# Optimization experiments

Hardware: AMD Instinct MI355X
Metric: run time of the kernel (lower is better)

The kernel has to match this reference:

```python
import jax, jax.numpy as jnp
import numpy as np

N_NODES, N_EDGES, BATCH, F_IN, GENES = 65536, 262144, 2048, 78, 735
HEADS, HID = 8, 64            # gnn_out_dim = HEADS*HID = 512
GOUT = HEADS * HID
NEG_SLOPE = 0.2
BN_EPS = 1e-5


def setup_inputs() -> dict:
    key = jax.random.key(0)
    ks = jax.random.split(key, 24)
    sc = lambda k, shp, fan: (jax.random.normal(k, shp, jnp.float32) / np.sqrt(fan)).astype(jnp.float32)
    d = {}
    d["x"] = jax.random.normal(ks[0], (N_NODES, F_IN), jnp.float32)
    d["edge_index"] = jax.random.randint(ks[1], (2, N_EDGES), 0, N_NODES)
    d["batch"] = jnp.sort(jax.random.randint(ks[2], (N_NODES,), 0, BATCH))
    d["x_gen"] = jax.random.normal(ks[3], (BATCH, GENES), jnp.float32)
    # GATConv 1: in=78 -> heads*hid
    d["W1"] = sc(ks[4], (F_IN, GOUT), F_IN)
    d["att_src1"] = sc(ks[5], (HEADS, HID), HID)
    d["att_dst1"] = sc(ks[6], (HEADS, HID), HID)
    d["bias1"] = jnp.zeros((GOUT,), jnp.float32)
    # GATConv 2: in=512 -> heads*hid
    d["W2"] = sc(ks[7], (GOUT, GOUT), GOUT)
    d["att_src2"] = sc(ks[8], (HEADS, HID), HID)
    d["att_dst2"] = sc(ks[9], (HEADS, HID), HID)
    d["bias2"] = jnp.zeros((GOUT,), jnp.float32)
    # geno encoder: Linear(735,128) -> BN -> ReLU -> Linear(128,512) -> ReLU
    d["gW1"] = sc(ks[10], (GENES, 2 * HID), GENES)
    d["gb1"] = jnp.zeros((2 * HID,), jnp.float32)
    d["bn_gamma"] = jnp.ones((2 * HID,), jnp.float32)
    d["bn_beta"] = jnp.zeros((2 * HID,), jnp.float32)
    d["bn_mean"] = jnp.zeros((2 * HID,), jnp.float32)
    d["bn_var"] = jnp.ones((2 * HID,), jnp.float32)
    d["gW2"] = sc(ks[11], (2 * HID, GOUT), 2 * HID)
    d["gb2"] = jnp.zeros((GOUT,), jnp.float32)
    # fusion MLP: 1024 -> 256 -> 128 -> 1
    d["fW1"] = sc(ks[12], (2 * GOUT, 256), 2 * GOUT)
    d["fb1"] = jnp.zeros((256,), jnp.float32)
    d["fW2"] = sc(ks[13], (256, 128), 256)
    d["fb2"] = jnp.zeros((128,), jnp.float32)
    d["fW3"] = sc(ks[14], (128, 1), 128)
    d["fb3"] = jnp.zeros((1,), jnp.float32)
    return d


def gat_layer(x, edge_index, W, att_src, att_dst, bias):
    """PyG GATConv (concat=True, add_self_loops=True), eval mode (no dropout)."""
    N = x.shape[0]
    H, C = att_src.shape
    h = (x @ W).reshape(N, H, C)                      # [N,H,C]
    a_src = jnp.einsum('nhc,hc->nh', h, att_src)      # [N,H]
    a_dst = jnp.einsum('nhc,hc->nh', h, att_dst)      # [N,H]
    loop = jnp.arange(N)
    src = jnp.concatenate([edge_index[0], loop])      # [E+N]
    dst = jnp.concatenate([edge_index[1], loop])
    e = jax.nn.leaky_relu(a_src[src] + a_dst[dst], NEG_SLOPE)   # [E+N,H]
    # scatter-softmax over incoming edges per destination node
    e_max = jax.ops.segment_max(e, dst, num_segments=N)
    e = jnp.exp(e - e_max[dst])
    denom = jax.ops.segment_sum(e, dst, num_segments=N)
    alpha = e / (denom[dst] + 1e-16)                  # [E+N,H]
    msg = h[src] * alpha[:, :, None]                  # [E+N,H,C]
    out = jax.ops.segment_sum(msg, dst, num_segments=N)  # [N,H,C]
    return out.reshape(N, H * C) + bias


def global_mean_pool(x, batch, num_graphs):
    sums = jax.ops.segment_sum(x, batch, num_segments=num_graphs)
    cnt = jax.ops.segment_sum(jnp.ones((x.shape[0],), x.dtype), batch, num_segments=num_graphs)
    return sums / jnp.maximum(cnt, 1.0)[:, None]


def reference(x, edge_index, batch, x_gen,
              W1, att_src1, att_dst1, bias1,
              W2, att_src2, att_dst2, bias2,
              gW1, gb1, bn_gamma, bn_beta, bn_mean, bn_var, gW2, gb2,
              fW1, fb1, fW2, fb2, fW3, fb3):
    h = jax.nn.elu(gat_layer(x, edge_index, W1, att_src1, att_dst1, bias1))
    h = jax.nn.elu(gat_layer(h, edge_index, W2, att_src2, att_dst2, bias2))
    g = global_mean_pool(h, batch, BATCH)             # [B, 512]
    # genomic encoder (eval-mode BatchNorm with running stats)
    z = x_gen @ gW1 + gb1
    z = (z - bn_mean) * jax.lax.rsqrt(bn_var + BN_EPS) * bn_gamma + bn_beta
    z = jax.nn.relu(z)
    z = jax.nn.relu(z @ gW2 + gb2)                    # [B, 512]
    c = jnp.concatenate([g, z], axis=1)               # [B, 1024]
    c = jax.nn.relu(c @ fW1 + fb1)
    c = jax.nn.relu(c @ fW2 + fb2)
    return c @ fW3 + fb3                              # [B, 1]
```

## Files before the change

kernel.cpp:

```cpp
#include <hip/hip_runtime.h>
#include <hip/hip_bf16.h>
#include <cstdint>
#include <cstddef>

#define NN 65536
#define NE 262144
#define NB 2048
#define FIN 78
#define GOUTD 512

typedef __bf16 bf16x8 __attribute__((ext_vector_type(8)));
typedef float f32x4 __attribute__((ext_vector_type(4)));

__device__ __forceinline__ float leaky02(float x) { return x > 0.f ? x : 0.2f * x; }

__global__ void k_zero2(int* __restrict__ a, int* __restrict__ b) {
    int i = blockIdx.x * 256 + threadIdx.x;
    if (i < NN) { a[i] = 0; b[i] = 0; }
}

__global__ void k_hist(const int* __restrict__ dst, int* __restrict__ deg) {
    int i = blockIdx.x * 256 + threadIdx.x;
    if (i < NE) atomicAdd(&deg[dst[i]], 1);
}

__global__ void k_scan_block(const int* __restrict__ deg, int* __restrict__ ex, int* __restrict__ bsum) {
    __shared__ int s[256];
    int t = threadIdx.x; int g = blockIdx.x * 256 + t;
    int v = deg[g];
    s[t] = v; __syncthreads();
    for (int d = 1; d < 256; d <<= 1) {
        int x = (t >= d) ? s[t - d] : 0;
        __syncthreads();
        s[t] += x;
        __syncthreads();
    }
    ex[g] = s[t] - v;
    if (t == 255) bsum[blockIdx.x] = s[t];
}

__global__ void k_scan_bsum(int* __restrict__ bsum) {
    __shared__ int s[256];
    int t = threadIdx.x;
    int v = bsum[t]; s[t] = v; __syncthreads();
    for (int d = 1; d < 256; d <<= 1) {
        int x = (t >= d) ? s[t - d] : 0;
        __syncthreads();
        s[t] += x;
        __syncthreads();
    }
    bsum[t] = s[t] - v;
}

__global__ void k_scan_add(int* __restrict__ rowptr, const int* __restrict__ bsum) {
    int i = blockIdx.x * 256 + threadIdx.x;
    rowptr[i] += bsum[blockIdx.x];
    if (i == 0) rowptr[NN] = NE;
}

__global__ void k_scatter(const int* __restrict__ src, const int* __restrict__ dst,
                          const int* __restrict__ rowptr, int* __restrict__ fill,
                          int* __restrict__ colI) {
    int i = blockIdx.x * 256 + threadIdx.x;
    if (i < NE) {
        int d = dst[i];
        int pos = rowptr[d] + atomicAdd(&fill[d], 1);
        colI[pos] = src[i];
    }
}

__global__ void k_gbounds(const int* __restrict__ batch, int* __restrict__ gstart) {
    int i = blockIdx.x * 256 + threadIdx.x;
    if (i >= NN) return;
    int cur = batch[i];
    int prev = (i == 0) ? -1 : batch[i - 1];
    for (int b = prev + 1; b <= cur; ++b) gstart[b] = i;
    if (i == NN - 1) {
        for (int b = cur + 1; b <= NB; ++b) gstart[b] = NN;
    }
}

__global__ void k_cvt_all(const float* __restrict__ x, const float* __restrict__ W1,
                          const float* __restrict__ W2, __hip_bfloat16* __restrict__ xb,
                          __hip_bfloat16* __restrict__ w1t, __hip_bfloat16* __restrict__ w2t)
{
    int blk = blockIdx.x;
    if (blk < 16384) {
        int i = blk * 256 + threadIdx.x;
        int row = i >> 6;
        int c = (i & 63) << 1;
        float v0 = (c < FIN) ? x[(size_t)row * FIN + c] : 0.f;
        float v1 = (c + 1 < FIN) ? x[(size_t)row * FIN + c + 1] : 0.f;
        __hip_bfloat16 o[2];
        o[0] = __float2bfloat16(v0);
        o[1] = __float2bfloat16(v1);
        *(uint32_t*)&xb[(size_t)row * 128 + c] = *(const uint32_t*)o;
    } else if (blk < 16640) {
        int i = (blk - 16384) * 256 + threadIdx.x;
        int n = i >> 7, k = i & 127;
        w1t[i] = __float2bfloat16(k < FIN ? W1[(size_t)k * 512 + n] : 0.f);
    } else {
        int i = (blk - 16640) * 256 + threadIdx.x;
        int n = i >> 9, k = i & 511;
        w2t[i] = __float2bfloat16(W2[(size_t)k * 512 + n]);
    }
}

__global__ __launch_bounds__(256) void k_mfma_gemm(
    const __hip_bfloat16* __restrict__ A, const __hip_bfloat16* __restrict__ BT,
    __hip_bfloat16* __restrict__ C, int K,
    const float* __restrict__ att_src, const float* __restrict__ att_dst,
    float* __restrict__ a_src, float* __restrict__ a_dst)
{
    __shared__ __hip_bfloat16 smem[128 * 128];
    __hip_bfloat16* As = smem;
    __hip_bfloat16* Bs = smem + 128 * 64;
    int tid = threadIdx.x;
    int lane = tid & 63;
    int wave = tid >> 6;
    int id = blockIdx.x;
    int m0 = (((id >> 5) << 3) + (id & 7)) * 128;
    int n0 = ((id >> 3) & 3) * 128;
    int wm = (wave >> 1) * 64;
    int wn = (wave & 1) * 64;
    f32x4 acc[4][4] = {};

    int swz = lane & 7;

    for (int k0 = 0; k0 < K; k0 += 64) {
        #pragma unroll
        for (int c = 0; c < 4; ++c) {
            int off = c * 4096 + tid * 16;
            int r = off >> 7;
            int c16 = (off >> 4) & 7;
            int c16s = c16 ^ (r & 7);
            __builtin_amdgcn_global_load_lds(
                (const __attribute__((address_space(1))) void*)(A + (size_t)(m0 + r) * K + k0 + c16s * 8),
                (__attribute__((address_space(3))) void*)((char*)As + off), 16, 0, 0);
            __builtin_amdgcn_global_load_lds(
                (const __attribute__((address_space(1))) void*)(BT + (size_t)(n0 + r) * K + k0 + c16s * 8),
                (__attribute__((address_space(3))) void*)((char*)Bs + off), 16, 0, 0);
        }
        __syncthreads();
        #pragma unroll
        for (int kk = 0; kk < 64; kk += 32) {
            int c16r = (kk >> 3) + (lane >> 4);
            bf16x8 af[4], bfr[4];
            #pragma unroll
            for (int t = 0; t < 4; ++t) {
                int ra = wm + t * 16 + (lane & 15);
                int rb = wn + t * 16 + (lane & 15);
                af[t]  = *(const bf16x8*)((char*)As + ra * 128 + ((c16r ^ swz) << 4));
                bfr[t] = *(const bf16x8*)((char*)Bs + rb * 128 + ((c16r ^ swz) << 4));
            }
            #pragma unroll
            for (int i = 0; i < 4; ++i)
                #pragma unroll
                for (int j = 0; j < 4; ++j)
                    acc[i][j] = __builtin_amdgcn_mfma_f32_16x16x32_bf16(af[i], bfr[j], acc[i][j], 0, 0, 0);
        }
        __syncthreads();
    }

    int rowb = wm + ((lane >> 4) << 2);
    int colb = wn + (lane & 15);
    #pragma unroll
    for (int i = 0; i < 4; ++i) {
        #pragma unroll
        for (int j = 0; j < 4; ++j) {
            int cc = colb + j * 16;
            #pragma unroll
            for (int r = 0; r < 4; ++r) {
                int rr = rowb + i * 16 + r;
                int word = (cc >> 1) ^ (((rr >> 2) & 7) << 3);
                smem[rr * 128 + word * 2 + (cc & 1)] = __float2bfloat16(acc[i][j][r]);
            }
        }
    }
    __syncthreads();
    #pragma unroll
    for (int cc2 = 0; cc2 < 8; ++cc2) {
        int p = cc2 * 256 + tid;
        int rr = p >> 4;
        int c16 = p & 15;
        int x = ((rr >> 2) & 7) << 3;
        bf16x8 v = *(const bf16x8*)((char*)smem + rr * 256 + ((((c16 << 2) ^ x)) << 2));
        *(bf16x8*)(C + (size_t)(m0 + rr) * 512 + n0 + c16 * 8) = v;
        const float* sp = att_src + n0 + c16 * 8;
        const float* dp = att_dst + n0 + c16 * 8;
        float4 s0 = *(const float4*)sp, s1 = *(const float4*)(sp + 4);
        float4 d0 = *(const float4*)dp, d1 = *(const float4*)(dp + 4);
        float sv[8] = {s0.x, s0.y, s0.z, s0.w, s1.x, s1.y, s1.z, s1.w};
        float dv[8] = {d0.x, d0.y, d0.z, d0.w, d1.x, d1.y, d1.z, d1.w};
        float ps = 0.f, pd = 0.f;
        #pragma unroll
        for (int k = 0; k < 8; ++k) {
            float f = (float)v[k];
            ps = fmaf(f, sv[k], ps);
            pd = fmaf(f, dv[k], pd);
        }
        #pragma unroll
        for (int d = 1; d < 8; d <<= 1) {
            ps += __shfl_xor(ps, d);
            pd += __shfl_xor(pd, d);
        }
        if ((c16 & 7) == 0) {
            int head = (n0 >> 6) + (c16 >> 3);
            a_src[(size_t)(m0 + rr) * 8 + head] = ps;
            a_dst[(size_t)(m0 + rr) * 8 + head] = pd;
        }
    }
}

__global__ __launch_bounds__(256) void k_geno1(
    const float* __restrict__ x_gen, const float* __restrict__ gW1,
    const float* __restrict__ gb1, const float* __restrict__ bn_mean,
    const float* __restrict__ bn_var, const float* __restrict__ bn_gamma,
    const float* __restrict__ bn_beta, float* __restrict__ z1)
{
    __shared__ float rowS[2][736];
    __shared__ float part[2][128];
    int t = threadIdx.x;
    int row0 = blockIdx.x * 2;
    int c = t & 127;
    int kh = t >> 7;
    for (int i = t; i < 1470; i += 256)
        rowS[i >= 735][i >= 735 ? i - 735 : i] = x_gen[(size_t)row0 * 735 + i];
    __syncthreads();
    int k0 = kh ? 368 : 0;
    int k1 = kh ? 735 : 368;
    float a0 = 0.f, a1 = 0.f;
    #pragma unroll 4
    for (int k = k0; k < k1; ++k) {
        float wv = gW1[(size_t)k * 128 + c];
        a0 = fmaf(rowS[0][k], wv, a0);
        a1 = fmaf(rowS[1][k], wv, a1);
    }
    if (kh) { part[0][c] = a0; part[1][c] = a1; }
    __syncthreads();
    if (!kh) {
        a0 += part[0][c];
        a1 += part[1][c];
        float sc = rsqrtf(bn_var[c] + 1e-5f) * bn_gamma[c];
        float sh = bn_beta[c] + (gb1[c] - bn_mean[c]) * sc;
        z1[(size_t)row0 * 128 + c]       = fmaxf(fmaf(a0, sc, sh), 0.f);
        z1[(size_t)(row0 + 1) * 128 + c] = fmaxf(fmaf(a1, sc, sh), 0.f);
    }
}

__global__ __launch_bounds__(256) void k_geno2(
    const float* __restrict__ z1, const float* __restrict__ gW2,
    const float* __restrict__ gb2, float* __restrict__ cbuf)
{
    __shared__ float zS[2][128];
    int t = threadIdx.x;
    int row0 = blockIdx.x * 2;
    if (t < 128) zS[0][t] = z1[(size_t)row0 * 128 + t];
    else zS[1][t - 128] = z1[(size_t)(row0 + 1) * 128 + (t - 128)];
    __syncthreads();
    int c = t << 1;
    float a00 = 0.f, a01 = 0.f, a10 = 0.f, a11 = 0.f;
    #pragma unroll 4
    for (int k = 0; k < 128; ++k) {
        float2 wv = *(const float2*)&gW2[(size_t)k * 512 + c];
        float z0 = zS[0][k], z1v = zS[1][k];
        a00 = fmaf(z0, wv.x, a00); a01 = fmaf(z0, wv.y, a01);
        a10 = fmaf(z1v, wv.x, a10); a11 = fmaf(z1v, wv.y, a11);
    }
    float2 g = *(const float2*)&gb2[c];
    float* op0 = cbuf + (size_t)row0 * 1024 + 512 + c;
    float* op1 = cbuf + (size_t)(row0 + 1) * 1024 + 512 + c;
    *(float2*)op0 = make_float2(fmaxf(a00 + g.x, 0.f), fmaxf(a01 + g.y, 0.f));
    *(float2*)op1 = make_float2(fmaxf(a10 + g.x, 0.f), fmaxf(a11 + g.y, 0.f));
}

__global__ __launch_bounds__(256) void k_gat_agg(
    const __hip_bfloat16* __restrict__ h, const float* __restrict__ asrc,
    const float* __restrict__ adst, const int* __restrict__ rowptr,
    const int* __restrict__ colI, const float* __restrict__ bias,
    __hip_bfloat16* __restrict__ out)
{
    int lane = threadIdx.x & 63;
    int n = blockIdx.x * 4 + (threadIdx.x >> 6);
    int start = rowptr[n], end = rowptr[n + 1];
    int hh = lane >> 3;
    float adst_h = adst[n * 8 + hh];
    float acc[8];
    float wsum;
    {
        float w = __expf(leaky02(asrc[n * 8 + hh] + adst_h));
        wsum = w;
        bf16x8 v = *(const bf16x8*)(h + (size_t)n * GOUTD + lane * 8);
        #pragma unroll
        for (int j = 0; j < 8; ++j) acc[j] = w * (float)v[j];
    }
    int i = start;
    for (; i + 1 < end; i += 2) {
        int s0 = colI[i];
        int s1 = colI[i + 1];
        float w0 = __expf(leaky02(asrc[s0 * 8 + hh] + adst_h));
        float w1 = __expf(leaky02(asrc[s1 * 8 + hh] + adst_h));
        bf16x8 v0 = *(const bf16x8*)(h + (size_t)s0 * GOUTD + lane * 8);
        bf16x8 v1 = *(const bf16x8*)(h + (size_t)s1 * GOUTD + lane * 8);
        wsum += w0 + w1;
        #pragma unroll
        for (int j = 0; j < 8; ++j)
            acc[j] = fmaf(w0, (float)v0[j], fmaf(w1, (float)v1[j], acc[j]));
    }
    if (i < end) {
        int s = colI[i];
        float w = __expf(leaky02(asrc[s * 8 + hh] + adst_h));
        wsum += w;
        bf16x8 v = *(const bf16x8*)(h + (size_t)s * GOUTD + lane * 8);
        #pragma unroll
        for (int j = 0; j < 8; ++j) acc[j] = fmaf(w, (float)v[j], acc[j]);
    }
    float rden = 1.f / (wsum + 1e-16f);
    const float* bp = bias + lane * 8;
    float4 b0 = *(const float4*)bp, b1 = *(const float4*)(bp + 4);
    float bb[8] = {b0.x, b0.y, b0.z, b0.w, b1.x, b1.y, b1.z, b1.w};
    __hip_bfloat16 o[8] __attribute__((aligned(16)));
    #pragma unroll
    for (int j = 0; j < 8; ++j) {
        float v = fmaf(acc[j], rden, bb[j]);
        v = (v > 0.f) ? v : (__expf(v) - 1.f);
        o[j] = __float2bfloat16(v);
    }
    *(bf16x8*)(out + (size_t)n * GOUTD + lane * 8) = *(const bf16x8*)o;
}

__global__ __launch_bounds__(256) void k_pool(
    const __hip_bfloat16* __restrict__ h, const int* __restrict__ gstart,
    float* __restrict__ cfeat)
{
    __shared__ float red[4][512];
    int b = blockIdx.x;
    int lane = threadIdx.x & 63;
    int wv = threadIdx.x >> 6;
    int s = gstart[b], e = gstart[b + 1];
    float acc[8] = {};
    for (int i = s + wv; i < e; i += 4) {
        bf16x8 v = *(const bf16x8*)(h + (size_t)i * GOUTD + lane * 8);
        #pragma unroll
        for (int j = 0; j < 8; ++j) acc[j] += (float)v[j];
    }
    #pragma unroll
    for (int j = 0; j < 8; ++j) red[wv][lane * 8 + j] = acc[j];
    __syncthreads();
    if (wv == 0) {
        float inv = 1.f / fmaxf((float)(e - s), 1.f);
        float* cp = cfeat + (size_t)b * 1024;
        #pragma unroll
        for (int j = 0; j < 8; ++j) {
            int c = lane * 8 + j;
            cp[c] = (red[0][c] + red[1][c] + red[2][c] + red[3][c]) * inv;
        }
    }
}

__global__ __launch_bounds__(256) void k_fgemm(
    const float* __restrict__ A, const float* __restrict__ B,
    const float* __restrict__ bias, float* __restrict__ C, int N, int K)
{
    __shared__ float As[16][32];
    __shared__ float Bs[16][64];
    int tid = threadIdx.x;
    int m0 = blockIdx.y * 32, n0 = blockIdx.x * 64;
    int tm = (tid >> 4) << 1;
    int tn = (tid & 15) << 2;
    int ar = tid >> 3;
    int ac = (tid & 7) << 1;
    int bk = tid >> 4;
    int bc = (tid & 15) << 2;
    float acc[2][4] = {};
    for (int k0 = 0; k0 < K; k0 += 16) {
        const float* ap = A + (size_t)(m0 + ar) * K + k0 + ac;
        As[ac][ar] = ap[0];
        As[ac + 1][ar] = ap[1];
        *(float4*)&Bs[bk][bc] = *(const float4*)(B + (size_t)(k0 + bk) * N + n0 + bc);
        __syncthreads();
        #pragma unroll
        for (int k = 0; k < 16; ++k) {
            float a0 = As[k][tm], a1 = As[k][tm + 1];
            float4 b4 = *(const float4*)&Bs[k][tn];
            acc[0][0] = fmaf(a0, b4.x, acc[0][0]); acc[0][1] = fmaf(a0, b4.y, acc[0][1]);
            acc[0][2] = fmaf(a0, b4.z, acc[0][2]); acc[0][3] = fmaf(a0, b4.w, acc[0][3]);
            acc[1][0] = fmaf(a1, b4.x, acc[1][0]); acc[1][1] = fmaf(a1, b4.y, acc[1][1]);
            acc[1][2] = fmaf(a1, b4.z, acc[1][2]); acc[1][3] = fmaf(a1, b4.w, acc[1][3]);
        }
        __syncthreads();
    }
    float4 bb = *(const float4*)&bias[n0 + tn];
    #pragma unroll
    for (int i = 0; i < 2; ++i) {
        int row = m0 + tm + i;
        float4 o = make_float4(fmaxf(acc[i][0] + bb.x, 0.f), fmaxf(acc[i][1] + bb.y, 0.f),
                               fmaxf(acc[i][2] + bb.z, 0.f), fmaxf(acc[i][3] + bb.w, 0.f));
        *(float4*)&C[(size_t)row * N + n0 + tn] = o;
    }
}

__global__ __launch_bounds__(256) void k_fout(
    const float* __restrict__ t2, const float* __restrict__ fW3,
    const float* __restrict__ fb3, float* __restrict__ out)
{
    int lane = threadIdx.x & 63;
    int row = blockIdx.x * 4 + (threadIdx.x >> 6);
    const float* tp = t2 + (size_t)row * 128;
    float p = tp[lane] * fW3[lane] + tp[lane + 64] * fW3[lane + 64];
    #pragma unroll
    for (int d = 1; d < 64; d <<= 1) p += __shfl_xor(p, d);
    if (lane == 0) out[row] = p + fb3[0];
}

extern "C" void kernel_launch(void* const* d_in, const int* in_sizes, int n_in,
                              void* d_out, int out_size, void* d_ws, size_t ws_size,
                              hipStream_t stream) {
    const float* x        = (const float*)d_in[0];
    const int*   ei       = (const int*)d_in[1];
    const int*   batch    = (const int*)d_in[2];
    const float* x_gen    = (const float*)d_in[3];
    const float* W1       = (const float*)d_in[4];
    const float* att_src1 = (const float*)d_in[5];
    const float* att_dst1 = (const float*)d_in[6];
    const float* bias1    = (const float*)d_in[7];
    const float* W2       = (const float*)d_in[8];
    const float* att_src2 = (const float*)d_in[9];
    const float* att_dst2 = (const float*)d_in[10];
    const float* bias2    = (const float*)d_in[11];
    const float* gW1      = (const float*)d_in[12];
    const float* gb1      = (const float*)d_in[13];
    const float* bn_gamma = (const float*)d_in[14];
    const float* bn_beta  = (const float*)d_in[15];
    const float* bn_mean  = (const float*)d_in[16];
    const float* bn_var   = (const float*)d_in[17];
    const float* gW2      = (const float*)d_in[18];
    const float* gb2      = (const float*)d_in[19];
    const float* fW1      = (const float*)d_in[20];
    const float* fb1      = (const float*)d_in[21];
    const float* fW2      = (const float*)d_in[22];
    const float* fb2      = (const float*)d_in[23];
    const float* fW3      = (const float*)d_in[24];
    const float* fb3      = (const float*)d_in[25];
    float* out = (float*)d_out;

    const int* srcv = ei;
    const int* dstv = ei + NE;

    char* w = (char*)d_ws;
    size_t off = 0;
    auto take = [&](size_t bytes) -> void* {
        void* p = w + off;
        off += (bytes + 255) & ~(size_t)255;
        return p;
    };
    __hip_bfloat16* hbuf = (__hip_bfloat16*)take((size_t)NN * GOUTD * 2);
    __hip_bfloat16* abuf = (__hip_bfloat16*)take((size_t)NN * GOUTD * 2);
    __hip_bfloat16* xb   = (__hip_bfloat16*)take((size_t)NN * 128 * 2);
    __hip_bfloat16* w1t  = (__hip_bfloat16*)take((size_t)512 * 128 * 2);
    __hip_bfloat16* w2t  = (__hip_bfloat16*)take((size_t)512 * 512 * 2);
    float* asrc   = (float*)take((size_t)NN * 8 * 4);
    float* adst   = (float*)take((size_t)NN * 8 * 4);
    int*   rowptr = (int*)take((size_t)(NN + 1) * 4);
    int*   colI   = (int*)take((size_t)NE * 4);
    int*   deg    = (int*)take((size_t)NN * 4);
    int*   fill   = (int*)take((size_t)NN * 4);
    int*   bsum   = (int*)take(256 * 4);
    int*   gstart = (int*)take((NB + 1) * 4);
    float* cbuf = (float*)xb;
    float* z1   = cbuf + (size_t)2048 * 1024;
    float* t1   = z1 + (size_t)2048 * 128;
    float* t2   = t1 + (size_t)2048 * 256;

    k_zero2<<<NN / 256, 256, 0, stream>>>(deg, fill);
    k_hist<<<NE / 256, 256, 0, stream>>>(dstv, deg);
    k_scan_block<<<256, 256, 0, stream>>>(deg, rowptr, bsum);
    k_scan_bsum<<<1, 256, 0, stream>>>(bsum);
    k_scan_add<<<256, 256, 0, stream>>>(rowptr, bsum);
    k_scatter<<<NE / 256, 256, 0, stream>>>(srcv, dstv, rowptr, fill, colI);
    k_gbounds<<<256, 256, 0, stream>>>(batch, gstart);
    k_cvt_all<<<17664, 256, 0, stream>>>(x, W1, W2, xb, w1t, w2t);

    k_mfma_gemm<<<2048, 256, 0, stream>>>(xb, w1t, hbuf, 128, att_src1, att_dst1, asrc, adst);
    k_gat_agg<<<NN / 4, 256, 0, stream>>>(hbuf, asrc, adst, rowptr, colI, bias1, abuf);

    k_mfma_gemm<<<2048, 256, 0, stream>>>(abuf, w2t, hbuf, 512, att_src2, att_dst2, asrc, adst);
    k_gat_agg<<<NN / 4, 256, 0, stream>>>(hbuf, asrc, adst, rowptr, colI, bias2, abuf);

    k_pool<<<NB, 256, 0, stream>>>(abuf, gstart, cbuf);
    k_geno1<<<NB / 2, 256, 0, stream>>>(x_gen, gW1, gb1, bn_mean, bn_var, bn_gamma, bn_beta, z1);
    k_geno2<<<NB / 2, 256, 0, stream>>>(z1, gW2, gb2, cbuf);

    k_fgemm<<<dim3(4, 64), 256, 0, stream>>>(cbuf, fW1, fb1, t1, 256, 1024);
    k_fgemm<<<dim3(2, 64), 256, 0, stream>>>(t1, fW2, fb2, t2, 128, 256);
    k_fout<<<NB / 4, 256, 0, stream>>>(t2, fW3, fb3, out);
}
```

Baseline: 485.9 us.

## Split-K the fusion MLP GEMMs with a separate bias+ReLU reduce kernel

Replaces the fusion-MLP fp32 GEMM kernel with a split-K variant that launches four K-slices per output tile, writing partial sums into the freed hbuf workspace. A new reduce kernel then sums the partials and applies bias and ReLU. The aim is more blocks for the small 2048-row GEMMs (256 and 128 blocks before) so more CUs are busy. It also widens the K tile to 32, uses vectorized A loads, and pads shared memory. The cost is two extra launches and extra partial-sum traffic through global memory.

```diff
diff --git a/kernel.cpp b/kernel.cpp
--- a/kernel.cpp
+++ b/kernel.cpp
@@ -358,46 +358,71 @@
     }
 }
 
-__global__ __launch_bounds__(256) void k_fgemm(
+#define FBM 32
+#define FBN 64
+#define FKS 32
+
+__global__ __launch_bounds__(256) void k_fgemm_sk(
     const float* __restrict__ A, const float* __restrict__ B,
-    const float* __restrict__ bias, float* __restrict__ C, int N, int K)
-{
-    __shared__ float As[16][32];
-    __shared__ float Bs[16][64];
+    float* __restrict__ P, int N, int K, int KS)
+{
+    __shared__ float As[FKS][FBM + 2];
+    __shared__ float Bs[FKS][FBN + 4];
     int tid = threadIdx.x;
-    int m0 = blockIdx.y * 32, n0 = blockIdx.x * 64;
+    int n0 = blockIdx.x * FBN;
+    int m0 = blockIdx.y * FBM;
+    int kbase = blockIdx.z * KS;
+    int am = tid >> 3;
+    int ak = (tid & 7) << 2;
+    int bk = tid >> 4;
+    int bc = (tid & 15) << 2;
     int tm = (tid >> 4) << 1;
     int tn = (tid & 15) << 2;
-    int ar = tid >> 3;
-    int ac = (tid & 7) << 1;
-    int bk = tid >> 4;
-    int bc = (tid & 15) << 2;
     float acc[2][4] = {};
-    for (int k0 = 0; k0 < K; k0 += 16) {
-        const float* ap = A + (size_t)(m0 + ar) * K + k0 + ac;
-        As[ac][ar] = ap[0];
-        As[ac + 1][ar] = ap[1];
-        *(float4*)&Bs[bk][bc] = *(const float4*)(B + (size_t)(k0 + bk) * N + n0 + bc);
-        __syncthreads();
-        #pragma unroll
-        for (int k = 0; k < 16; ++k) {
-            float a0 = As[k][tm], a1 = As[k][tm + 1];
-            float4 b4 = *(const float4*)&Bs[k][tn];
-            acc[0][0] = fmaf(a0, b4.x, acc[0][0]); acc[0][1] = fmaf(a0, b4.y, acc[0][1]);
-            acc[0][2] = fmaf(a0, b4.z, acc[0][2]); acc[0][3] = fmaf(a0, b4.w, acc[0][3]);
-            acc[1][0] = fmaf(a1, b4.x, acc[1][0]); acc[1][1] = fmaf(a1, b4.y, acc[1][1]);
-            acc[1][2] = fmaf(a1, b4.z, acc[1][2]); acc[1][3] = fmaf(a1, b4.w, acc[1][3]);
-        }
-        __syncthreads();
-    }
-    float4 bb = *(const float4*)&bias[n0 + tn];
+    for (int kt = 0; kt < KS; kt += FKS) {
+        float4 a4 = *(const float4*)(A + (size_t)(m0 + am) * K + kbase + kt + ak);
+        As[ak][am] = a4.x; As[ak + 1][am] = a4.y;
+        As[ak + 2][am] = a4.z; As[ak + 3][am] = a4.w;
+        #pragma unroll
+        for (int j = 0; j < 2; ++j) {
+            int kr = j * 16 + bk;
+            *(float4*)&Bs[kr][bc] = *(const float4*)(B + (size_t)(kbase + kt + kr) * N + n0 + bc);
+        }
+        __syncthreads();
+        #pragma unroll
+        for (int kk = 0; kk < FKS; ++kk) {
+            float2 a2 = *(const float2*)&As[kk][tm];
+            float4 b4 = *(const float4*)&Bs[kk][tn];
+            acc[0][0] = fmaf(a2.x, b4.x, acc[0][0]); acc[0][1] = fmaf(a2.x, b4.y, acc[0][1]);
+            acc[0][2] = fmaf(a2.x, b4.z, acc[0][2]); acc[0][3] = fmaf(a2.x, b4.w, acc[0][3]);
+            acc[1][0] = fmaf(a2.y, b4.x, acc[1][0]); acc[1][1] = fmaf(a2.y, b4.y, acc[1][1]);
+            acc[1][2] = fmaf(a2.y, b4.z, acc[1][2]); acc[1][3] = fmaf(a2.y, b4.w, acc[1][3]);
+        }
+        __syncthreads();
+    }
     #pragma unroll
     for (int i = 0; i < 2; ++i) {
-        int row = m0 + tm + i;
-        float4 o = make_float4(fmaxf(acc[i][0] + bb.x, 0.f), fmaxf(acc[i][1] + bb.y, 0.f),
-                               fmaxf(acc[i][2] + bb.z, 0.f), fmaxf(acc[i][3] + bb.w, 0.f));
-        *(float4*)&C[(size_t)row * N + n0 + tn] = o;
-    }
+        float4 o = make_float4(acc[i][0], acc[i][1], acc[i][2], acc[i][3]);
+        *(float4*)(P + ((size_t)blockIdx.z * NB + m0 + tm + i) * N + n0 + tn) = o;
+    }
+}
+
+__global__ __launch_bounds__(256) void k_freduce(
+    const float* __restrict__ P, const float* __restrict__ bias,
+    float* __restrict__ C, int N)
+{
+    int i4 = blockIdx.x * 256 + threadIdx.x;
+    int base = i4 << 2;
+    int col = base & (N - 1);
+    size_t stride = (size_t)NB * N;
+    float4 v = *(const float4*)&bias[col];
+    #pragma unroll
+    for (int s = 0; s < 4; ++s) {
+        float4 p = *(const float4*)&P[s * stride + base];
+        v.x += p.x; v.y += p.y; v.z += p.z; v.w += p.w;
+    }
+    *(float4*)&C[base] = make_float4(fmaxf(v.x, 0.f), fmaxf(v.y, 0.f),
+                                     fmaxf(v.z, 0.f), fmaxf(v.w, 0.f));
 }
 
 __global__ __launch_bounds__(256) void k_fout(
@@ -471,6 +496,7 @@
     float* z1   = cbuf + (size_t)2048 * 1024;
     float* t1   = z1 + (size_t)2048 * 128;
     float* t2   = t1 + (size_t)2048 * 256;
+    float* fpart = (float*)hbuf;
 
     k_zero2<<<NN / 256, 256, 0, stream>>>(deg, fill);
     k_hist<<<NE / 256, 256, 0, stream>>>(dstv, deg);
@@ -491,7 +517,9 @@
     k_geno1<<<NB / 2, 256, 0, stream>>>(x_gen, gW1, gb1, bn_mean, bn_var, bn_gamma, bn_beta, z1);
     k_geno2<<<NB / 2, 256, 0, stream>>>(z1, gW2, gb2, cbuf);
 
-    k_fgemm<<<dim3(4, 64), 256, 0, stream>>>(cbuf, fW1, fb1, t1, 256, 1024);
-    k_fgemm<<<dim3(2, 64), 256, 0, stream>>>(t1, fW2, fb2, t2, 128, 256);
+    k_fgemm_sk<<<dim3(4, 64, 4), 256, 0, stream>>>(cbuf, fW1, fpart, 256, 1024, 256);
+    k_freduce<<<512, 256, 0, stream>>>(fpart, fb1, t1, 256);
+    k_fgemm_sk<<<dim3(2, 64, 4), 256, 0, stream>>>(t1, fW2, fpart, 128, 256, 64);
+    k_freduce<<<256, 256, 0, stream>>>(fpart, fb2, t2, 128);
     k_fout<<<NB / 4, 256, 0, stream>>>(t2, fW3, fb3, out);
 }
```

After: 461.9 us. 4.9% less time.
